# Optimization experiments

Measured on AMD Instinct MI355X. Metric: run time of the kernel, lower is better.

Reference implementation:

```python
import jax, jax.numpy as jnp
import numpy as np

B, T, HID = 16, 512, 1024
NH, NKV, D = 8, 4, 128
THETA = 10000.0


def setup_inputs() -> dict:
    key = jax.random.key(0)
    k0, k1, k2, k3, k4 = jax.random.split(key, 5)
    s = 0.02
    return {
        "hidden_states": jax.random.normal(k0, (B, T, HID), dtype=jnp.float32),
        "Wq": s * jax.random.normal(k1, (HID, NH * D), dtype=jnp.float32),
        "Wk": s * jax.random.normal(k2, (HID, NKV * D), dtype=jnp.float32),
        "Wv": s * jax.random.normal(k3, (HID, NKV * D), dtype=jnp.float32),
        "Wo": s * jax.random.normal(k4, (NH * D, HID), dtype=jnp.float32),
    }


def _rotate_half(x):
    x1, x2 = x[..., : x.shape[-1] // 2], x[..., x.shape[-1] // 2:]
    return jnp.concatenate((-x2, x1), axis=-1)


def reference(hidden_states, Wq, Wk, Wv, Wo):
    b, t, _ = hidden_states.shape
    # projections -> [B, H, T, D]
    q = (hidden_states @ Wq).reshape(b, t, NH, D).transpose(0, 2, 1, 3)
    k = (hidden_states @ Wk).reshape(b, t, NKV, D).transpose(0, 2, 1, 3)
    v = (hidden_states @ Wv).reshape(b, t, NKV, D).transpose(0, 2, 1, 3)

    # RoPE: cos/sin [T, D]
    inv_freq = 1.0 / (THETA ** (jnp.arange(0, D, 2, dtype=jnp.float32) / D))
    freqs = jnp.outer(jnp.arange(t, dtype=jnp.float32), inv_freq)
    emb = jnp.concatenate((freqs, freqs), axis=-1)
    cos, sin = jnp.cos(emb), jnp.sin(emb)
    q = q * cos + _rotate_half(q) * sin
    k = k * cos + _rotate_half(k) * sin

    # repeat_interleave KV heads to match query heads (GQA)
    groups = NH // NKV
    k = jnp.repeat(k, groups, axis=1)  # [B, NH, T, D]
    v = jnp.repeat(v, groups, axis=1)

    scale = 1.0 / jnp.sqrt(jnp.float32(D))
    attn = jnp.einsum("bhtd,bhsd->bhts", q, k) * scale  # [B, NH, T, T]
    causal = jnp.triu(jnp.ones((t, t), dtype=bool), k=1)
    attn = jnp.where(causal, -jnp.inf, attn)
    attn = jax.nn.softmax(attn, axis=-1)  # dropout p=0 (eval)

    out = jnp.einsum("bhts,bhsd->bhtd", attn, v)
    out = out.transpose(0, 2, 1, 3).reshape(b, t, NH * D)
    return out @ Wo  # [B, T, HID]
```

## Files before the change

### kernel.cpp

```cpp
#include <hip/hip_runtime.h>
#include <hip/hip_bf16.h>
#include <math.h>

#define Bn 16
#define Tn 512
#define HIDn 1024
#define NHn 8
#define NKVn 4
#define Dn 128

typedef __attribute__((ext_vector_type(8))) short short8;
typedef __attribute__((ext_vector_type(4))) float floatx4;

__device__ __forceinline__ short bf16r(float f) {
  __hip_bfloat16 h = __float2bfloat16(f);
  return *(short*)&h;
}
__device__ __forceinline__ float bf16f(short s) {
  __hip_bfloat16 h = *(__hip_bfloat16*)&s;
  return __bfloat162float(h);
}

__device__ __forceinline__ void g2l16(const short* g, short* l) {
  __builtin_amdgcn_global_load_lds(
      (const __attribute__((address_space(1))) void*)g,
      (__attribute__((address_space(3))) void*)l, 16, 0, 0);
}

__global__ __launch_bounds__(256) void prep_kernel(const float* __restrict__ X,
                                                   const float* __restrict__ Wq,
                                                   const float* __restrict__ Wk,
                                                   const float* __restrict__ Wv,
                                                   const float* __restrict__ Wo,
                                                   short* __restrict__ Xb,
                                                   short* __restrict__ BtQKV,
                                                   short* __restrict__ Wot) {
  __shared__ float tile[32][33];
  int bid = blockIdx.x;
  if (bid < 4096) {
    int i = bid * 256 + threadIdx.x;
    const float4* p = reinterpret_cast<const float4*>(X) + (size_t)i * 2;
    float4 a = p[0], b = p[1];
    short8 o;
    o[0] = bf16r(a.x); o[1] = bf16r(a.y); o[2] = bf16r(a.z); o[3] = bf16r(a.w);
    o[4] = bf16r(b.x); o[5] = bf16r(b.y); o[6] = bf16r(b.z); o[7] = bf16r(b.w);
    reinterpret_cast<short8*>(Xb)[i] = o;
    return;
  }
  int t = bid - 4096;
  const float* in;
  short* out;
  int N;
  if (t < 1024)      { in = Wq; out = BtQKV;               N = 1024; }
  else if (t < 1536) { t -= 1024; in = Wk; out = BtQKV + 1024 * 1024; N = 512; }
  else if (t < 2048) { t -= 1536; in = Wv; out = BtQKV + 1536 * 1024; N = 512; }
  else               { t -= 2048; in = Wo; out = Wot;                N = 1024; }
  int ntx = N >> 5;
  int n0 = (t % ntx) * 32, k0 = (t / ntx) * 32;
  int tx = threadIdx.x & 31, ty = threadIdx.x >> 5;
  for (int i = 0; i < 32; i += 8)
    tile[ty + i][tx] = in[(size_t)(k0 + ty + i) * N + n0 + tx];
  __syncthreads();
  for (int i = 0; i < 32; i += 8)
    out[(size_t)(n0 + ty + i) * 1024 + k0 + tx] = bf16r(tile[tx][ty + i]);
}

template <bool OUTF32>
__global__ __launch_bounds__(256) void gemm_bt(const short* __restrict__ A,
                                               const short* __restrict__ Bt,
                                               void* __restrict__ Cout,
                                               int M, int N, int K) {
  __shared__ __align__(16) short As[128 * 64];
  __shared__ __align__(16) short Bs[128 * 64];
  const int tid = threadIdx.x;
  const int wave = tid >> 6, lane = tid & 63;
  const int quad = lane >> 4, l16 = lane & 15;
  const int wrow = wave >> 1, wcol = wave & 1;
  const int m0 = blockIdx.y * 128, n0 = blockIdx.x * 128;
  floatx4 acc[4][4];
  for (int mi = 0; mi < 4; ++mi)
    for (int ni = 0; ni < 4; ++ni)
      acc[mi][ni] = (floatx4){0.f, 0.f, 0.f, 0.f};

  for (int kt = 0; kt < K; kt += 64) {
#pragma unroll
    for (int v = 0; v < 4; ++v) {
      int s = tid + v * 256;
      int r = s >> 3;
      int c = (s & 7) ^ (r & 7);
      short* dstA = (short*)As + (size_t)(v * 256 + wave * 64) * 8;
      g2l16(&A[(size_t)(m0 + r) * K + kt + c * 8], dstA);
      short* dstB = (short*)Bs + (size_t)(v * 256 + wave * 64) * 8;
      g2l16(&Bt[(size_t)(n0 + r) * K + kt + c * 8], dstB);
    }
    __syncthreads();
#pragma unroll
    for (int kc = 0; kc < 2; ++kc) {
      short8 af[4], bfr[4];
#pragma unroll
      for (int mi = 0; mi < 4; ++mi) {
        int R = wrow * 64 + mi * 16 + l16;
        int pos = (kc * 4 + quad) ^ (R & 7);
        af[mi] = *(short8*)&As[R * 64 + pos * 8];
      }
#pragma unroll
      for (int ni = 0; ni < 4; ++ni) {
        int R = wcol * 64 + ni * 16 + l16;
        int pos = (kc * 4 + quad) ^ (R & 7);
        bfr[ni] = *(short8*)&Bs[R * 64 + pos * 8];
      }
#pragma unroll
      for (int mi = 0; mi < 4; ++mi)
#pragma unroll
        for (int ni = 0; ni < 4; ++ni)
          acc[mi][ni] = __builtin_amdgcn_mfma_f32_16x16x32_bf16(af[mi], bfr[ni], acc[mi][ni], 0, 0, 0);
    }
    __syncthreads();
  }
#pragma unroll
  for (int mi = 0; mi < 4; ++mi)
#pragma unroll
    for (int ni = 0; ni < 4; ++ni)
#pragma unroll
      for (int r = 0; r < 4; ++r) {
        int row = m0 + wrow * 64 + mi * 16 + quad * 4 + r;
        int col = n0 + wcol * 64 + ni * 16 + l16;
        if (OUTF32)
          ((float*)Cout)[(size_t)row * N + col] = acc[mi][ni][r];
        else
          ((short*)Cout)[(size_t)row * N + col] = bf16r(acc[mi][ni][r]);
      }
}

template <bool OUTF32>
__global__ __launch_bounds__(256) void gemm_bt64(const short* __restrict__ A,
                                                 const short* __restrict__ Bt,
                                                 void* __restrict__ Cout,
                                                 int M, int N, int K) {
  __shared__ __align__(16) short As[128 * 64];
  __shared__ __align__(16) short Bs[64 * 64];
  const int tid = threadIdx.x;
  const int wave = tid >> 6, lane = tid & 63;
  const int quad = lane >> 4, l16 = lane & 15;
  const int wrow = wave >> 1, wcol = wave & 1;
  const int m0 = blockIdx.y * 128, n0 = blockIdx.x * 64;
  floatx4 acc[4][2];
  for (int mi = 0; mi < 4; ++mi)
    for (int ni = 0; ni < 2; ++ni)
      acc[mi][ni] = (floatx4){0.f, 0.f, 0.f, 0.f};

  for (int kt = 0; kt < K; kt += 64) {
#pragma unroll
    for (int v = 0; v < 4; ++v) {
      int s = tid + v * 256;
      int r = s >> 3;
      int c = (s & 7) ^ (r & 7);
      short* dstA = (short*)As + (size_t)(v * 256 + wave * 64) * 8;
      g2l16(&A[(size_t)(m0 + r) * K + kt + c * 8], dstA);
    }
#pragma unroll
    for (int v = 0; v < 2; ++v) {
      int s = tid + v * 256;
      int r = s >> 3;
      int c = (s & 7) ^ (r & 7);
      short* dstB = (short*)Bs + (size_t)(v * 256 + wave * 64) * 8;
      g2l16(&Bt[(size_t)(n0 + r) * K + kt + c * 8], dstB);
    }
    __syncthreads();
#pragma unroll
    for (int kc = 0; kc < 2; ++kc) {
      short8 af[4], bfr[2];
#pragma unroll
      for (int mi = 0; mi < 4; ++mi) {
        int R = wrow * 64 + mi * 16 + l16;
        int pos = (kc * 4 + quad) ^ (R & 7);
        af[mi] = *(short8*)&As[R * 64 + pos * 8];
      }
#pragma unroll
      for (int ni = 0; ni < 2; ++ni) {
        int R = wcol * 32 + ni * 16 + l16;
        int pos = (kc * 4 + quad) ^ (R & 7);
        bfr[ni] = *(short8*)&Bs[R * 64 + pos * 8];
      }
#pragma unroll
      for (int mi = 0; mi < 4; ++mi)
#pragma unroll
        for (int ni = 0; ni < 2; ++ni)
          acc[mi][ni] = __builtin_amdgcn_mfma_f32_16x16x32_bf16(af[mi], bfr[ni], acc[mi][ni], 0, 0, 0);
    }
    __syncthreads();
  }
#pragma unroll
  for (int mi = 0; mi < 4; ++mi)
#pragma unroll
    for (int ni = 0; ni < 2; ++ni)
#pragma unroll
      for (int r = 0; r < 4; ++r) {
        int row = m0 + wrow * 64 + mi * 16 + quad * 4 + r;
        int col = n0 + wcol * 32 + ni * 16 + l16;
        if (OUTF32)
          ((float*)Cout)[(size_t)row * N + col] = acc[mi][ni][r];
        else
          ((short*)Cout)[(size_t)row * N + col] = bf16r(acc[mi][ni][r]);
      }
}

__global__ __launch_bounds__(256) void ropev_kernel(short* __restrict__ C,
                                                    short* __restrict__ Vt) {
  __shared__ short tile[32][33];
  int bid = blockIdx.x;
  if (bid < 1024) {
    int idx = bid * 256 + threadIdx.x;
    int vec = idx & 7;
    int head = (idx >> 3) & 3;
    int bt = idx >> 5;
    int t = bt & (Tn - 1);
    int i0 = vec * 8;
    size_t base = (size_t)bt * 2048 + 1024 + head * 128 + i0;
    short8 x1 = *(short8*)&C[base];
    short8 x2 = *(short8*)&C[base + 64];
    short8 o1, o2;
    float tf = (float)t;
#pragma unroll
    for (int j = 0; j < 8; ++j) {
      float a = tf * exp2f(-0.2076205059f * (float)(i0 + j));
      float s, c;
      sincosf(a, &s, &c);
      float v1 = bf16f(x1[j]), v2 = bf16f(x2[j]);
      o1[j] = bf16r(v1 * c - v2 * s);
      o2[j] = bf16r(v2 * c + v1 * s);
    }
    *(short8*)&C[base] = o1;
    *(short8*)&C[base + 64] = o2;
    return;
  }
  int i = bid - 1024;
  int t0 = (i & 15) * 32, d0 = ((i >> 4) & 3) * 32, bkv = i >> 6;
  int b = bkv >> 2, kv = bkv & 3;
  int tx = threadIdx.x & 31, ty = threadIdx.x >> 5;
  const short* src = C + (size_t)b * Tn * 2048 + 1536 + kv * 128;
  for (int j = 0; j < 32; j += 8)
    tile[ty + j][tx] = src[(size_t)(t0 + ty + j) * 2048 + d0 + tx];
  __syncthreads();
  short* dst = Vt + ((size_t)(b * NKVn + kv) * 128 + d0) * Tn + t0;
  for (int j = 0; j < 32; j += 8)
    dst[(size_t)(ty + j) * Tn + tx] = tile[tx][ty + j];
}

__global__ __launch_bounds__(256) void attn_kernel(const short* __restrict__ Cqkv,
                                                   const short* __restrict__ Vt,
                                                   short* __restrict__ Aout) {
  __shared__ __align__(16) short Ks[64 * 128];
  __shared__ __align__(16) short Vs[128 * 64];
  __shared__ short Ps[4][16][72];
  const int tid = threadIdx.x;
  const int wave = tid >> 6, lane = tid & 63;
  const int quad = lane >> 4, l16 = lane & 15;
  const int blk = blockIdx.x;
  const int qt = 7 - (blk >> 7);
  const int h = blk & 7, b = (blk >> 3) & 15;
  const int kvh = h >> 1;
  const short* Qp = Cqkv + (size_t)b * Tn * 2048 + h * 128;
  const short* Kp = Cqkv + (size_t)b * Tn * 2048 + 1024 + kvh * 128;
  const short* Vtp = Vt + (size_t)(b * NKVn + kvh) * 128 * Tn;

  const int qrow0 = qt * 64 + wave * 16;
  const float scale = 0.08838834764831845f;

  short8 qf[4];
#pragma unroll
  for (int kc = 0; kc < 4; ++kc)
    qf[kc] = *(const short8*)&Qp[(size_t)(qrow0 + l16) * 2048 + kc * 32 + quad * 8];
  {
    float tf = (float)(qrow0 + l16);
#pragma unroll
    for (int kc = 0; kc < 2; ++kc)
#pragma unroll
      for (int j = 0; j < 8; ++j) {
        int d = kc * 32 + quad * 8 + j;
        float a = tf * exp2f(-0.2076205059f * (float)d);
        float s, c;
        sincosf(a, &s, &c);
        float x1 = bf16f(qf[kc][j]), x2 = bf16f(qf[kc + 2][j]);
        qf[kc][j] = bf16r((x1 * c - x2 * s) * scale);
        qf[kc + 2][j] = bf16r((x2 * c + x1 * s) * scale);
      }
  }

  floatx4 o[8];
  float l_part[4];
#pragma unroll
  for (int ni = 0; ni < 8; ++ni) o[ni] = (floatx4){0.f, 0.f, 0.f, 0.f};
#pragma unroll
  for (int r = 0; r < 4; ++r) l_part[r] = 0.f;

  const int nk = qt * 64 + 64;

  for (int k0 = 0; k0 < nk; k0 += 64) {
#pragma unroll
    for (int v = 0; v < 4; ++v) {
      int s = tid + v * 256;
      int r = s >> 4, c = (s & 15) ^ (r & 15);
      short* dstK = (short*)Ks + (size_t)(v * 256 + wave * 64) * 8;
      g2l16(&Kp[(size_t)(k0 + r) * 2048 + c * 8], dstK);
    }
#pragma unroll
    for (int v = 0; v < 4; ++v) {
      int s = tid + v * 256;
      int r = s >> 3, c = (s & 7) ^ (r & 7);
      short* dstV = (short*)Vs + (size_t)(v * 256 + wave * 64) * 8;
      g2l16(&Vtp[(size_t)r * Tn + k0 + c * 8], dstV);
    }
    __syncthreads();

    floatx4 s[4];
#pragma unroll
    for (int ni = 0; ni < 4; ++ni) {
      s[ni] = (floatx4){0.f, 0.f, 0.f, 0.f};
      short8 kf[4];
#pragma unroll
      for (int kc = 0; kc < 4; ++kc) {
        int R = ni * 16 + l16;
        int pos = (kc * 4 + quad) ^ (R & 15);
        kf[kc] = *(short8*)&Ks[R * 128 + pos * 8];
      }
#pragma unroll
      for (int kc = 0; kc < 4; ++kc)
        s[ni] = __builtin_amdgcn_mfma_f32_16x16x32_bf16(qf[kc], kf[kc], s[ni], 0, 0, 0);
    }

    const bool diag = (k0 + 63 > qrow0);
#pragma unroll
    for (int ni = 0; ni < 4; ++ni)
#pragma unroll
      for (int r = 0; r < 4; ++r) {
        float p = __expf(s[ni][r]);
        if (diag) {
          int key = k0 + ni * 16 + l16;
          int qr = qrow0 + quad * 4 + r;
          if (key > qr) p = 0.f;
        }
        s[ni][r] = p;
        l_part[r] += p;
      }

#pragma unroll
    for (int ni = 0; ni < 4; ++ni)
#pragma unroll
      for (int r = 0; r < 4; ++r)
        Ps[wave][quad * 4 + r][ni * 16 + l16] = bf16r(s[ni][r]);

    short8 pf[2];
#pragma unroll
    for (int kc = 0; kc < 2; ++kc)
      pf[kc] = *(short8*)&Ps[wave][l16][kc * 32 + quad * 8];
#pragma unroll
    for (int ni = 0; ni < 8; ++ni) {
      int R = ni * 16 + l16;
      int pos0 = quad ^ (R & 7);
      int pos1 = (4 + quad) ^ (R & 7);
      short8 vf0 = *(short8*)&Vs[R * 64 + pos0 * 8];
      short8 vf1 = *(short8*)&Vs[R * 64 + pos1 * 8];
      o[ni] = __builtin_amdgcn_mfma_f32_16x16x32_bf16(pf[0], vf0, o[ni], 0, 0, 0);
      o[ni] = __builtin_amdgcn_mfma_f32_16x16x32_bf16(pf[1], vf1, o[ni], 0, 0, 0);
    }
    __syncthreads();
  }

  float inv[4];
#pragma unroll
  for (int r = 0; r < 4; ++r) {
    float rs = l_part[r];
#pragma unroll
    for (int off = 8; off >= 1; off >>= 1) rs += __shfl_xor(rs, off, 16);
    inv[r] = 1.0f / rs;
  }
#pragma unroll
  for (int ni = 0; ni < 8; ++ni)
#pragma unroll
    for (int r = 0; r < 4; ++r) {
      int t = qrow0 + quad * 4 + r;
      int d = ni * 16 + l16;
      Aout[((size_t)b * Tn + t) * 1024 + h * 128 + d] = bf16r(o[ni][r] * inv[r]);
    }
}

extern "C" void kernel_launch(void* const* d_in, const int* in_sizes, int n_in,
                              void* d_out, int out_size, void* d_ws, size_t ws_size,
                              hipStream_t stream) {
  const float* X  = (const float*)d_in[0];
  const float* Wq = (const float*)d_in[1];
  const float* Wk = (const float*)d_in[2];
  const float* Wv = (const float*)d_in[3];
  const float* Wo = (const float*)d_in[4];

  char* ws = (char*)d_ws;
  short* Xb    = (short*)(ws);
  short* BtQKV = (short*)(ws + (16ull << 20));
  short* Wot   = (short*)(ws + (20ull << 20));
  short* Cqkv  = (short*)(ws + (22ull << 20));
  short* Vt    = (short*)(ws + (54ull << 20));
  short* Aout  = (short*)(ws + (62ull << 20));

  prep_kernel<<<7168, 256, 0, stream>>>(X, Wq, Wk, Wv, Wo, Xb, BtQKV, Wot);
  gemm_bt<false><<<dim3(16, 64), 256, 0, stream>>>(Xb, BtQKV, Cqkv, 8192, 2048, 1024);
  ropev_kernel<<<5120, 256, 0, stream>>>(Cqkv, Vt);
  attn_kernel<<<1024, 256, 0, stream>>>(Cqkv, Vt, Aout);
  gemm_bt64<true><<<dim3(16, 64), 256, 0, stream>>>(Aout, Wot, d_out, 8192, 1024, 1024);
}
```

Measured before the change: 201.6 us.

## Fuse RoPE and V transpose into QKV GEMM epilogue; use 128-wide output GEMM

Adds a QKV projection GEMM whose epilogue applies RoPE to the K columns and writes V transposed through shared memory. This removes the separate ropev kernel and its extra global read and write of K and V. The output projection also moves from the 64-wide-N GEMM to the 128x128 tile GEMM, which halves the block count. The trade-off is larger tiles and more epilogue work per block, with some lost parallelism in the final GEMM.

```diff
diff --git a/kernel.cpp b/kernel.cpp
--- a/kernel.cpp
+++ b/kernel.cpp
@@ -65,6 +65,128 @@
     out[(size_t)(n0 + ty + i) * 1024 + k0 + tx] = bf16r(tile[tx][ty + i]);
 }
 
+__global__ __launch_bounds__(256) void gemm_qkv(const short* __restrict__ A,
+                                                const short* __restrict__ Bt,
+                                                short* __restrict__ Cqkv,
+                                                short* __restrict__ Vt) {
+  __shared__ __align__(16) short SH[128 * 136];
+  short* As = SH;
+  short* Bs = SH + 128 * 64;
+  const int K = 1024, N = 2048;
+  const int tid = threadIdx.x;
+  const int wave = tid >> 6, lane = tid & 63;
+  const int quad = lane >> 4, l16 = lane & 15;
+  const int wrow = wave >> 1, wcol = wave & 1;
+  const int m0 = blockIdx.y * 128, n0 = blockIdx.x * 128;
+  floatx4 acc[4][4];
+  for (int mi = 0; mi < 4; ++mi)
+    for (int ni = 0; ni < 4; ++ni)
+      acc[mi][ni] = (floatx4){0.f, 0.f, 0.f, 0.f};
+
+  for (int kt = 0; kt < K; kt += 64) {
+#pragma unroll
+    for (int v = 0; v < 4; ++v) {
+      int s = tid + v * 256;
+      int r = s >> 3;
+      int c = (s & 7) ^ (r & 7);
+      short* dstA = As + (size_t)(v * 256 + wave * 64) * 8;
+      g2l16(&A[(size_t)(m0 + r) * K + kt + c * 8], dstA);
+      short* dstB = Bs + (size_t)(v * 256 + wave * 64) * 8;
+      g2l16(&Bt[(size_t)(n0 + r) * K + kt + c * 8], dstB);
+    }
+    __syncthreads();
+#pragma unroll
+    for (int kc = 0; kc < 2; ++kc) {
+      short8 af[4], bfr[4];
+#pragma unroll
+      for (int mi = 0; mi < 4; ++mi) {
+        int R = wrow * 64 + mi * 16 + l16;
+        int pos = (kc * 4 + quad) ^ (R & 7);
+        af[mi] = *(short8*)&As[R * 64 + pos * 8];
+      }
+#pragma unroll
+      for (int ni = 0; ni < 4; ++ni) {
+        int R = wcol * 64 + ni * 16 + l16;
+        int pos = (kc * 4 + quad) ^ (R & 7);
+        bfr[ni] = *(short8*)&Bs[R * 64 + pos * 8];
+      }
+#pragma unroll
+      for (int mi = 0; mi < 4; ++mi)
+#pragma unroll
+        for (int ni = 0; ni < 4; ++ni)
+          acc[mi][ni] = __builtin_amdgcn_mfma_f32_16x16x32_bf16(af[mi], bfr[ni], acc[mi][ni], 0, 0, 0);
+    }
+    __syncthreads();
+  }
+
+  const int bx = blockIdx.x;
+  if (bx < 8) {
+#pragma unroll
+    for (int mi = 0; mi < 4; ++mi)
+#pragma unroll
+      for (int ni = 0; ni < 4; ++ni)
+#pragma unroll
+        for (int r = 0; r < 4; ++r) {
+          int row = m0 + wrow * 64 + mi * 16 + quad * 4 + r;
+          int col = n0 + wcol * 64 + ni * 16 + l16;
+          Cqkv[(size_t)row * N + col] = bf16r(acc[mi][ni][r]);
+        }
+  } else if (bx < 12) {
+#pragma unroll
+    for (int mi = 0; mi < 4; ++mi)
+#pragma unroll
+      for (int ni = 0; ni < 4; ++ni)
+#pragma unroll
+        for (int r = 0; r < 4; ++r) {
+          int tl = wrow * 64 + mi * 16 + quad * 4 + r;
+          int cl = wcol * 64 + ni * 16 + l16;
+          SH[tl * 136 + cl] = bf16r(acc[mi][ni][r]);
+        }
+    __syncthreads();
+#pragma unroll
+    for (int k2 = 0; k2 < 4; ++k2) {
+      int c = k2 * 256 + tid;
+      int row = c >> 3, d0 = (c & 7) << 3;
+      float tf = (float)((m0 + row) & (Tn - 1));
+      short8 x1 = *(short8*)&SH[row * 136 + d0];
+      short8 x2 = *(short8*)&SH[row * 136 + d0 + 64];
+      short8 o1, o2;
+#pragma unroll
+      for (int j = 0; j < 8; ++j) {
+        float a = tf * exp2f(-0.2076205059f * (float)(d0 + j));
+        float s, cc;
+        sincosf(a, &s, &cc);
+        float v1 = bf16f(x1[j]), v2 = bf16f(x2[j]);
+        o1[j] = bf16r(v1 * cc - v2 * s);
+        o2[j] = bf16r(v2 * cc + v1 * s);
+      }
+      size_t base = (size_t)(m0 + row) * N + n0 + d0;
+      *(short8*)&Cqkv[base] = o1;
+      *(short8*)&Cqkv[base + 64] = o2;
+    }
+  } else {
+#pragma unroll
+    for (int mi = 0; mi < 4; ++mi)
+#pragma unroll
+      for (int ni = 0; ni < 4; ++ni)
+#pragma unroll
+        for (int r = 0; r < 4; ++r) {
+          int tl = wrow * 64 + mi * 16 + quad * 4 + r;
+          int dl = wcol * 64 + ni * 16 + l16;
+          SH[dl * 136 + tl] = bf16r(acc[mi][ni][r]);
+        }
+    __syncthreads();
+    int kv = bx - 12, b = m0 >> 9, t0 = m0 & (Tn - 1);
+#pragma unroll
+    for (int k2 = 0; k2 < 8; ++k2) {
+      int c = k2 * 256 + tid;
+      int d = c >> 4, toff = (c & 15) << 3;
+      short8 v = *(short8*)&SH[d * 136 + toff];
+      *(short8*)&Vt[((size_t)(b * NKVn + kv) * 128 + d) * Tn + t0 + toff] = v;
+    }
+  }
+}
+
 template <bool OUTF32>
 __global__ __launch_bounds__(256) void gemm_bt(const short* __restrict__ A,
                                                const short* __restrict__ Bt,
@@ -132,121 +254,6 @@
       }
 }
 
-template <bool OUTF32>
-__global__ __launch_bounds__(256) void gemm_bt64(const short* __restrict__ A,
-                                                 const short* __restrict__ Bt,
-                                                 void* __restrict__ Cout,
-                                                 int M, int N, int K) {
-  __shared__ __align__(16) short As[128 * 64];
-  __shared__ __align__(16) short Bs[64 * 64];
-  const int tid = threadIdx.x;
-  const int wave = tid >> 6, lane = tid & 63;
-  const int quad = lane >> 4, l16 = lane & 15;
-  const int wrow = wave >> 1, wcol = wave & 1;
-  const int m0 = blockIdx.y * 128, n0 = blockIdx.x * 64;
-  floatx4 acc[4][2];
-  for (int mi = 0; mi < 4; ++mi)
-    for (int ni = 0; ni < 2; ++ni)
-      acc[mi][ni] = (floatx4){0.f, 0.f, 0.f, 0.f};
-
-  for (int kt = 0; kt < K; kt += 64) {
-#pragma unroll
-    for (int v = 0; v < 4; ++v) {
-      int s = tid + v * 256;
-      int r = s >> 3;
-      int c = (s & 7) ^ (r & 7);
-      short* dstA = (short*)As + (size_t)(v * 256 + wave * 64) * 8;
-      g2l16(&A[(size_t)(m0 + r) * K + kt + c * 8], dstA);
-    }
-#pragma unroll
-    for (int v = 0; v < 2; ++v) {
-      int s = tid + v * 256;
-      int r = s >> 3;
-      int c = (s & 7) ^ (r & 7);
-      short* dstB = (short*)Bs + (size_t)(v * 256 + wave * 64) * 8;
-      g2l16(&Bt[(size_t)(n0 + r) * K + kt + c * 8], dstB);
-    }
-    __syncthreads();
-#pragma unroll
-    for (int kc = 0; kc < 2; ++kc) {
-      short8 af[4], bfr[2];
-#pragma unroll
-      for (int mi = 0; mi < 4; ++mi) {
-        int R = wrow * 64 + mi * 16 + l16;
-        int pos = (kc * 4 + quad) ^ (R & 7);
-        af[mi] = *(short8*)&As[R * 64 + pos * 8];
-      }
-#pragma unroll
-      for (int ni = 0; ni < 2; ++ni) {
-        int R = wcol * 32 + ni * 16 + l16;
-        int pos = (kc * 4 + quad) ^ (R & 7);
-        bfr[ni] = *(short8*)&Bs[R * 64 + pos * 8];
-      }
-#pragma unroll
-      for (int mi = 0; mi < 4; ++mi)
-#pragma unroll
-        for (int ni = 0; ni < 2; ++ni)
-          acc[mi][ni] = __builtin_amdgcn_mfma_f32_16x16x32_bf16(af[mi], bfr[ni], acc[mi][ni], 0, 0, 0);
-    }
-    __syncthreads();
-  }
-#pragma unroll
-  for (int mi = 0; mi < 4; ++mi)
-#pragma unroll
-    for (int ni = 0; ni < 2; ++ni)
-#pragma unroll
-      for (int r = 0; r < 4; ++r) {
-        int row = m0 + wrow * 64 + mi * 16 + quad * 4 + r;
-        int col = n0 + wcol * 32 + ni * 16 + l16;
-        if (OUTF32)
-          ((float*)Cout)[(size_t)row * N + col] = acc[mi][ni][r];
-        else
-          ((short*)Cout)[(size_t)row * N + col] = bf16r(acc[mi][ni][r]);
-      }
-}
-
-__global__ __launch_bounds__(256) void ropev_kernel(short* __restrict__ C,
-                                                    short* __restrict__ Vt) {
-  __shared__ short tile[32][33];
-  int bid = blockIdx.x;
-  if (bid < 1024) {
-    int idx = bid * 256 + threadIdx.x;
-    int vec = idx & 7;
-    int head = (idx >> 3) & 3;
-    int bt = idx >> 5;
-    int t = bt & (Tn - 1);
-    int i0 = vec * 8;
-    size_t base = (size_t)bt * 2048 + 1024 + head * 128 + i0;
-    short8 x1 = *(short8*)&C[base];
-    short8 x2 = *(short8*)&C[base + 64];
-    short8 o1, o2;
-    float tf = (float)t;
-#pragma unroll
-    for (int j = 0; j < 8; ++j) {
-      float a = tf * exp2f(-0.2076205059f * (float)(i0 + j));
-      float s, c;
-      sincosf(a, &s, &c);
-      float v1 = bf16f(x1[j]), v2 = bf16f(x2[j]);
-      o1[j] = bf16r(v1 * c - v2 * s);
-      o2[j] = bf16r(v2 * c + v1 * s);
-    }
-    *(short8*)&C[base] = o1;
-    *(short8*)&C[base + 64] = o2;
-    return;
-  }
-  int i = bid - 1024;
-  int t0 = (i & 15) * 32, d0 = ((i >> 4) & 3) * 32, bkv = i >> 6;
-  int b = bkv >> 2, kv = bkv & 3;
-  int tx = threadIdx.x & 31, ty = threadIdx.x >> 5;
-  const short* src = C + (size_t)b * Tn * 2048 + 1536 + kv * 128;
-  for (int j = 0; j < 32; j += 8)
-    tile[ty + j][tx] = src[(size_t)(t0 + ty + j) * 2048 + d0 + tx];
-  __syncthreads();
-  short* dst = Vt + ((size_t)(b * NKVn + kv) * 128 + d0) * Tn + t0;
-  for (int j = 0; j < 32; j += 8)
-    dst[(size_t)(ty + j) * Tn + tx] = tile[tx][ty + j];
-}
-
 __global__ __launch_bounds__(256) void attn_kernel(const short* __restrict__ Cqkv,
                                                    const short* __restrict__ Vt,
                                                    short* __restrict__ Aout) {
@@ -403,8 +410,7 @@
   short* Aout  = (short*)(ws + (62ull << 20));
 
   prep_kernel<<<7168, 256, 0, stream>>>(X, Wq, Wk, Wv, Wo, Xb, BtQKV, Wot);
-  gemm_bt<false><<<dim3(16, 64), 256, 0, stream>>>(Xb, BtQKV, Cqkv, 8192, 2048, 1024);
-  ropev_kernel<<<5120, 256, 0, stream>>>(Cqkv, Vt);
+  gemm_qkv<<<dim3(16, 64), 256, 0, stream>>>(Xb, BtQKV, Cqkv, Vt);
   attn_kernel<<<1024, 256, 0, stream>>>(Cqkv, Vt, Aout);
-  gemm_bt64<true><<<dim3(16, 64), 256, 0, stream>>>(Aout, Wot, d_out, 8192, 1024, 1024);
-}
+  gemm_bt<true><<<dim3(8, 64), 256, 0, stream>>>(Aout, Wot, d_out, 8192, 1024, 1024);
+}
```

Result: no change. 199.3 us (-1.2%).
